# Kernel optimization log

Hardware: AMD Instinct MI355X
Metric: run time of the kernel (lower is better)

Reference implementation:

```python
import jax, jax.numpy as jnp
import numpy as np

H, W = 480, 640
NUM_CLASSES = 3
SKIP = 5            # skip_pixels: stride between voting pixels
GRID = 8            # stride of Hough accumulator bins
LABEL_THRESHOLD = 5
INLIER_THRESHOLD = 0.5
VOTING_THRESHOLD = 0.3


def setup_inputs():
    key = jax.random.key(0)
    k1, k2, k3, k4 = jax.random.split(key, 4)
    bottom_label = jax.random.randint(k1, (1, H, W), 0, NUM_CLASSES).astype(jnp.int32)
    bottom_vertex = jax.random.normal(k2, (1, NUM_CLASSES * 3, H, W), jnp.float32)
    bottom_meta_data = jax.random.normal(k3, (1, 10), jnp.float32)
    extents = jax.random.normal(k4, (NUM_CLASSES, 3), jnp.float32)
    return {"bottom_label": bottom_label, "bottom_vertex": bottom_vertex,
            "bottom_meta_data": bottom_meta_data, "extents": extents}


def _hough_voting(bottom_label, bottom_vertex, bottom_meta_data, extents):
    label = bottom_label[0]                                   # [H,W] int
    vert = bottom_vertex[0].reshape(NUM_CLASSES, 3, H, W)     # per-class (ux,uy,dist)

    # voter pixels on a SKIP-strided grid
    vy, vx = jnp.meshgrid(jnp.arange(0, H, SKIP), jnp.arange(0, W, SKIP), indexing="ij")
    vy = vy.reshape(-1)
    vx = vx.reshape(-1)                                       # [V]
    vl = label[vy, vx]                                        # voter class labels [V]
    d = vert[vl, :, vy, vx]                                   # [V,3] gather own-class prediction
    ux, uy, dist = d[:, 0], d[:, 1], d[:, 2]

    # Hough bin centers on a GRID-strided grid
    by, bx = jnp.meshgrid(jnp.arange(GRID // 2, H, GRID), jnp.arange(GRID // 2, W, GRID), indexing="ij")
    by = by.reshape(-1).astype(jnp.float32)
    bx = bx.reshape(-1).astype(jnp.float32)                   # [B]

    # per (voter, bin) agreement between predicted direction and vector to bin
    ddx = bx[None, :] - vx[:, None].astype(jnp.float32)       # [V,B]
    ddy = by[None, :] - vy[:, None].astype(jnp.float32)
    inv_n = jax.lax.rsqrt(ddx * ddx + ddy * ddy + 1e-6)
    cos = (ddx * ux[:, None] + ddy * uy[:, None]) * inv_n     # [V,B]
    w = jnp.where((cos > INLIER_THRESHOLD) & (vl[:, None] > 0), 1.0, 0.0)

    # scatter votes into per-class Hough space (class 0 = background, masked above)
    hough = jax.ops.segment_sum(w, vl, num_segments=NUM_CLASSES)                 # [C,B]
    dsum = jax.ops.segment_sum(w * dist[:, None], vl, num_segments=NUM_CLASSES)  # [C,B]
    counts = jax.ops.segment_sum(jnp.ones_like(vl, jnp.float32), vl, num_segments=NUM_CLASSES)

    # peak detection per class
    peak = jnp.argmax(hough, axis=1)                          # [C]
    votes = jnp.take_along_axis(hough, peak[:, None], axis=1)[:, 0]
    depth = jnp.take_along_axis(dsum, peak[:, None], axis=1)[:, 0] / jnp.maximum(votes, 1.0)
    cx = bx[peak]
    cy = by[peak]
    score = votes / jnp.maximum(counts, 1.0)
    valid = (counts > LABEL_THRESHOLD) & (score > VOTING_THRESHOLD)

    # project object extents through camera intrinsics at estimated depth -> box size
    fx = bottom_meta_data[0, 0]
    fy = bottom_meta_data[0, 4]
    diag = jnp.sqrt(jnp.sum(extents * extents, axis=1))       # [C]
    safe_z = jnp.maximum(jnp.abs(depth), 1e-3)
    bw = jnp.abs(diag * fx) / safe_z
    bh = jnp.abs(diag * fy) / safe_z

    cls = jnp.arange(NUM_CLASSES, dtype=jnp.float32)
    rois = jnp.stack([cls, cx - bw / 2, cy - bh / 2, cx + bw / 2, cy + bh / 2,
                      score * valid.astype(jnp.float32)], axis=1)  # [C,6]
    return rois, hough


def reference(bottom_label, bottom_vertex, bottom_meta_data, extents):
    return _hough_voting(bottom_label, bottom_vertex, bottom_meta_data, extents)
```

## Files before the change

kernel.cpp:

```cpp
#include <hip/hip_runtime.h>

#define HH 480
#define WW 640
#define NC 3
#define NVX 128
#define NVY 96
#define NV (NVX * NVY)
#define NBX 80
#define NBY 60
#define NB (NBX * NBY)
#define NPB 96
#define BKT 128
#define XBLK 10

__global__ void precompute_pts(const int* __restrict__ label,
                               const float* __restrict__ vert,
                               float4* __restrict__ ptsA,
                               float4* __restrict__ ptsB,
                               int* __restrict__ cnt,
                               float* __restrict__ blockCounts,
                               float* __restrict__ hough,
                               float* __restrict__ dsum) {
    __shared__ int swtot[2], sn2[2];
    const int tid = threadIdx.x;
    const int i = blockIdx.x * BKT + tid;
    const int iy = i >> 7;
    const int ix = i & (NVX - 1);
    const int pix = (5 * iy) * WW + 5 * ix;
    const int vl = label[pix];
    const float* base = vert + (size_t)(vl * 3) * HH * WW + pix;
    const float ux = base[0];
    const float uy = base[(size_t)HH * WW];
    const float dist = base[(size_t)2 * HH * WW];

    const bool pos = (vl > 0);
    const int lane = tid & 63, w = tid >> 6;
    unsigned long long mp = __ballot(pos);
    unsigned long long m2 = __ballot(vl == 2);
    int rank = __popcll(mp & ((1ull << lane) - 1ull));
    if (lane == 0) { swtot[w] = __popcll(mp); sn2[w] = __popcll(m2); }
    __syncthreads();
    if (pos) {
        int p = blockIdx.x * BKT + (w ? swtot[0] : 0) + rank;
        ptsA[p] = make_float4((float)(5 * ix), (float)(5 * iy), ux, uy);
        ptsB[p] = make_float4((vl == 1) ? dist : 0.0f,
                              (vl == 2) ? dist : 0.0f,
                              (vl == 1) ? 1.0f : 0.0f,
                              (vl == 2) ? 1.0f : 0.0f);
    }
    if (tid == 0) {
        int tot = swtot[0] + swtot[1];
        int n2 = sn2[0] + sn2[1];
        cnt[blockIdx.x] = tot;
        blockCounts[blockIdx.x * NC + 0] = (float)(BKT - tot);
        blockCounts[blockIdx.x * NC + 1] = (float)(tot - n2);
        blockCounts[blockIdx.x * NC + 2] = (float)n2;
    }
    for (int k = i; k < NC * NB; k += NV) hough[k] = 0.0f;
    if (i < 2 * NB) dsum[i] = 0.0f;
}

__global__ void vote(const float4* __restrict__ ptsA,
                     const float4* __restrict__ ptsB,
                     const int* __restrict__ cnt,
                     float* __restrict__ hough,
                     float* __restrict__ dsum) {
    __shared__ float4 shA[BKT];
    __shared__ float4 shB[BKT];
    const int tid = threadIdx.x;
    const int p0 = blockIdx.y * BKT;
    if (tid < BKT) shA[tid] = ptsA[p0 + tid];
    else           shB[tid - BKT] = ptsB[p0 + tid - BKT];
    const int n = cnt[blockIdx.y];

    const int b0 = 2 * (blockIdx.x * 256 + tid);
    const float bx0 = (float)(4 + 8 * (b0 % NBX));
    const float bx1 = bx0 + 8.0f;
    const float byf = (float)(4 + 8 * (b0 / NBX));
    float h10 = 0.f, h20 = 0.f, d10 = 0.f, d20 = 0.f;
    float h11 = 0.f, h21 = 0.f, d11 = 0.f, d21 = 0.f;
    float flagacc = -1.0f;
    __syncthreads();

    for (int j = 0; j < n; ++j) {
        float4 a = shA[j];
        float4 q = shB[j];
        float ddy = byf - a.y;
        float dyt = __builtin_fmaf(ddy, ddy, 1e-6f);
        float dyu = ddy * a.w;

        float ddx0 = bx0 - a.x;
        float nx0  = __builtin_fmaf(ddx0, ddx0, dyt);
        float dot0 = __builtin_fmaf(ddx0, a.z, dyu);
        float s0   = __builtin_fmaf(dot0, dot0, -0.25f * nx0);
        float g0   = fminf(dot0, s0);
        float f0   = fminf(dot0, __builtin_fmaf(nx0, 1e-6f, -fabsf(s0)));

        float ddx1 = bx1 - a.x;
        float nx1  = __builtin_fmaf(ddx1, ddx1, dyt);
        float dot1 = __builtin_fmaf(ddx1, a.z, dyu);
        float s1   = __builtin_fmaf(dot1, dot1, -0.25f * nx1);
        float g1   = fminf(dot1, s1);
        float f1   = fminf(dot1, __builtin_fmaf(nx1, 1e-6f, -fabsf(s1)));

        flagacc = fmaxf(flagacc, fmaxf(f0, f1));
        float m0 = (g0 > 0.0f) ? 1.0f : 0.0f;
        float m1 = (g1 > 0.0f) ? 1.0f : 0.0f;
        d10 = __builtin_fmaf(m0, q.x, d10);
        d20 = __builtin_fmaf(m0, q.y, d20);
        h10 = __builtin_fmaf(m0, q.z, h10);
        h20 = __builtin_fmaf(m0, q.w, h20);
        d11 = __builtin_fmaf(m1, q.x, d11);
        d21 = __builtin_fmaf(m1, q.y, d21);
        h11 = __builtin_fmaf(m1, q.z, h11);
        h21 = __builtin_fmaf(m1, q.w, h21);
    }

    if (b0 >= NB) flagacc = -1.0f;
    if (flagacc > 0.0f) {
        for (int j = 0; j < n; ++j) {
            float4 a = shA[j];
            float4 q = shB[j];
            float ddy = byf - a.y;
            float dyt = __builtin_fmaf(ddy, ddy, 1e-6f);
            float dyu = ddy * a.w;
#pragma unroll
            for (int k = 0; k < 2; ++k) {
                float bx = k ? bx1 : bx0;
                float ddx = bx - a.x;
                float nx  = __builtin_fmaf(ddx, ddx, dyt);
                float dot = __builtin_fmaf(ddx, a.z, dyu);
                float s   = __builtin_fmaf(dot, dot, -0.25f * nx);
                float mf  = (fminf(dot, s) > 0.0f) ? 1.0f : 0.0f;
                float nxe  = __fadd_rn(__fadd_rn(__fmul_rn(ddx, ddx),
                                                 __fmul_rn(ddy, ddy)), 1e-6f);
                float inve = __fdiv_rn(1.0f, __fsqrt_rn(nxe));
                float dote = __fadd_rn(__fmul_rn(ddx, a.z), __fmul_rn(ddy, a.w));
                float me   = (__fmul_rn(dote, inve) > 0.5f) ? 1.0f : 0.0f;
                float dm   = me - mf;
                if (k == 0) {
                    d10 = __builtin_fmaf(dm, q.x, d10);
                    d20 = __builtin_fmaf(dm, q.y, d20);
                    h10 = __builtin_fmaf(dm, q.z, h10);
                    h20 = __builtin_fmaf(dm, q.w, h20);
                } else {
                    d11 = __builtin_fmaf(dm, q.x, d11);
                    d21 = __builtin_fmaf(dm, q.y, d21);
                    h11 = __builtin_fmaf(dm, q.z, h11);
                    h21 = __builtin_fmaf(dm, q.w, h21);
                }
            }
        }
    }

    if (b0 < NB) {
        atomicAdd(&hough[NB + b0], h10);
        atomicAdd(&hough[2 * NB + b0], h20);
        atomicAdd(&dsum[b0], d10);
        atomicAdd(&dsum[NB + b0], d20);
        atomicAdd(&hough[NB + b0 + 1], h11);
        atomicAdd(&hough[2 * NB + b0 + 1], h21);
        atomicAdd(&dsum[b0 + 1], d11);
        atomicAdd(&dsum[NB + b0 + 1], d21);
    }
}

__global__ void finalize(const float* __restrict__ hough,
                         const float* __restrict__ dsum,
                         const float* __restrict__ blockCounts,
                         const float* __restrict__ meta,
                         const float* __restrict__ extents,
                         float* __restrict__ rois) {
    __shared__ unsigned long long skey[256];
    __shared__ float scnt[256];
    const int tid = threadIdx.x;
    const int c = blockIdx.x;

    float cntv = 0.0f;
    for (int i = tid; i < NPB; i += 256) cntv += blockCounts[i * NC + c];
    scnt[tid] = cntv;

    unsigned long long best = 0ull;
    for (int i = tid; i < NB; i += 256) {
        float v = hough[c * NB + i];
        unsigned long long key =
            ((unsigned long long)__float_as_uint(v) << 32) |
            (unsigned long long)(unsigned)(NB - 1 - i);
        if (key > best) best = key;
    }
    skey[tid] = best;
    __syncthreads();
    for (int s = 128; s > 0; s >>= 1) {
        if (tid < s) {
            if (skey[tid + s] > skey[tid]) skey[tid] = skey[tid + s];
            scnt[tid] += scnt[tid + s];
        }
        __syncthreads();
    }
    if (tid == 0) {
        float votes = __uint_as_float((unsigned)(skey[0] >> 32));
        int peak = NB - 1 - (int)(skey[0] & 0xffffffffull);
        float ds = (c == 0) ? 0.0f : dsum[(c - 1) * NB + peak];
        float depth = __fdiv_rn(ds, fmaxf(votes, 1.0f));
        float cx = (float)(4 + 8 * (peak % NBX));
        float cy = (float)(4 + 8 * (peak / NBX));
        float cntf = scnt[0];
        float score = __fdiv_rn(votes, fmaxf(cntf, 1.0f));
        int valid = (cntf > 5.0f) && (score > 0.3f);
        float fx = meta[0], fy = meta[4];
        float e0 = extents[c * 3 + 0];
        float e1 = extents[c * 3 + 1];
        float e2 = extents[c * 3 + 2];
        float diag = __fsqrt_rn(__fadd_rn(
            __fadd_rn(__fmul_rn(e0, e0), __fmul_rn(e1, e1)), __fmul_rn(e2, e2)));
        float sz = fmaxf(fabsf(depth), 0.001f);
        float bw = __fdiv_rn(fabsf(__fmul_rn(diag, fx)), sz);
        float bh = __fdiv_rn(fabsf(__fmul_rn(diag, fy)), sz);
        rois[c * 6 + 0] = (float)c;
        rois[c * 6 + 1] = cx - bw * 0.5f;
        rois[c * 6 + 2] = cy - bh * 0.5f;
        rois[c * 6 + 3] = cx + bw * 0.5f;
        rois[c * 6 + 4] = cy + bh * 0.5f;
        rois[c * 6 + 5] = valid ? score : 0.0f;
    }
}

extern "C" void kernel_launch(void* const* d_in, const int* in_sizes, int n_in,
                              void* d_out, int out_size, void* d_ws, size_t ws_size,
                              hipStream_t stream) {
    const int* label = (const int*)d_in[0];
    const float* vert = (const float*)d_in[1];
    const float* meta = (const float*)d_in[2];
    const float* extents = (const float*)d_in[3];
    float* out = (float*)d_out;

    char* ws = (char*)d_ws;
    float4* ptsA = (float4*)ws;
    float4* ptsB = (float4*)(ws + (size_t)NV * 16);
    float* dsum = (float*)(ws + (size_t)2 * NV * 16);
    float* blockCounts = (float*)(ws + (size_t)2 * NV * 16 + 2 * NB * 4);
    int* cnt = (int*)(ws + (size_t)2 * NV * 16 + 2 * NB * 4 + NPB * NC * 4);

    float* hough = out + NC * 6;

    precompute_pts<<<NPB, BKT, 0, stream>>>(label, vert, ptsA, ptsB,
                                            cnt, blockCounts, hough, dsum);
    vote<<<dim3(XBLK, NPB), 256, 0, stream>>>(ptsA, ptsB, cnt, hough, dsum);
    finalize<<<NC, 256, 0, stream>>>(hough, dsum, blockCounts, meta, extents, out);
}
```

Before: 113.0 us.

## Use 2x2 bin tiles per thread and replace atomics with partial-sum reduction

Each vote thread now handles a 2x2 block of Hough bins instead of a 1x2 pair, so the per-voter dy terms are reused across rows and only 5 x-blocks are launched. Global float atomics are replaced by per-voter-block partial planes written with float2 stores, and a new reduce kernel sums them. The zeroing of the hough and dsum buffers moves out of precompute into the reduce step. The cost is an extra kernel launch and roughly 7 MB of partial-buffer traffic, plus fewer threads in the vote kernel.

```diff
diff --git a/kernel.cpp b/kernel.cpp
--- a/kernel.cpp
+++ b/kernel.cpp
@@ -11,16 +11,15 @@
 #define NB (NBX * NBY)
 #define NPB 96
 #define BKT 128
-#define XBLK 10
+#define NLANE 1200
+#define XBLK 5
 
 __global__ void precompute_pts(const int* __restrict__ label,
                                const float* __restrict__ vert,
                                float4* __restrict__ ptsA,
                                float4* __restrict__ ptsB,
                                int* __restrict__ cnt,
-                               float* __restrict__ blockCounts,
-                               float* __restrict__ hough,
-                               float* __restrict__ dsum) {
+                               float* __restrict__ blockCounts) {
     __shared__ int swtot[2], sn2[2];
     const int tid = threadIdx.x;
     const int i = blockIdx.x * BKT + tid;
@@ -56,15 +55,12 @@
         blockCounts[blockIdx.x * NC + 1] = (float)(tot - n2);
         blockCounts[blockIdx.x * NC + 2] = (float)n2;
     }
-    for (int k = i; k < NC * NB; k += NV) hough[k] = 0.0f;
-    if (i < 2 * NB) dsum[i] = 0.0f;
 }
 
 __global__ void vote(const float4* __restrict__ ptsA,
                      const float4* __restrict__ ptsB,
                      const int* __restrict__ cnt,
-                     float* __restrict__ hough,
-                     float* __restrict__ dsum) {
+                     float* __restrict__ partial) {
     __shared__ float4 shA[BKT];
     __shared__ float4 shB[BKT];
     const int tid = threadIdx.x;
@@ -73,96 +69,115 @@
     else           shB[tid - BKT] = ptsB[p0 + tid - BKT];
     const int n = cnt[blockIdx.y];
 
-    const int b0 = 2 * (blockIdx.x * 256 + tid);
-    const float bx0 = (float)(4 + 8 * (b0 % NBX));
-    const float bx1 = bx0 + 8.0f;
-    const float byf = (float)(4 + 8 * (b0 / NBX));
-    float h10 = 0.f, h20 = 0.f, d10 = 0.f, d20 = 0.f;
-    float h11 = 0.f, h21 = 0.f, d11 = 0.f, d21 = 0.f;
+    const int gi = blockIdx.x * 256 + tid;
+    const int xp = gi % 40;
+    const int yp = gi / 40;
+    const float bx0 = (float)(4 + 16 * xp), bx1 = bx0 + 8.0f;
+    const float by0 = (float)(4 + 16 * yp), by1 = by0 + 8.0f;
+
+    float hh1[4] = {0.f, 0.f, 0.f, 0.f};
+    float hh2[4] = {0.f, 0.f, 0.f, 0.f};
+    float dd1[4] = {0.f, 0.f, 0.f, 0.f};
+    float dd2[4] = {0.f, 0.f, 0.f, 0.f};
     float flagacc = -1.0f;
     __syncthreads();
 
+#pragma unroll 2
     for (int j = 0; j < n; ++j) {
         float4 a = shA[j];
         float4 q = shB[j];
-        float ddy = byf - a.y;
-        float dyt = __builtin_fmaf(ddy, ddy, 1e-6f);
-        float dyu = ddy * a.w;
-
-        float ddx0 = bx0 - a.x;
-        float nx0  = __builtin_fmaf(ddx0, ddx0, dyt);
-        float dot0 = __builtin_fmaf(ddx0, a.z, dyu);
-        float s0   = __builtin_fmaf(dot0, dot0, -0.25f * nx0);
-        float g0   = fminf(dot0, s0);
-        float f0   = fminf(dot0, __builtin_fmaf(nx0, 1e-6f, -fabsf(s0)));
-
-        float ddx1 = bx1 - a.x;
-        float nx1  = __builtin_fmaf(ddx1, ddx1, dyt);
-        float dot1 = __builtin_fmaf(ddx1, a.z, dyu);
-        float s1   = __builtin_fmaf(dot1, dot1, -0.25f * nx1);
-        float g1   = fminf(dot1, s1);
-        float f1   = fminf(dot1, __builtin_fmaf(nx1, 1e-6f, -fabsf(s1)));
-
-        flagacc = fmaxf(flagacc, fmaxf(f0, f1));
-        float m0 = (g0 > 0.0f) ? 1.0f : 0.0f;
-        float m1 = (g1 > 0.0f) ? 1.0f : 0.0f;
-        d10 = __builtin_fmaf(m0, q.x, d10);
-        d20 = __builtin_fmaf(m0, q.y, d20);
-        h10 = __builtin_fmaf(m0, q.z, h10);
-        h20 = __builtin_fmaf(m0, q.w, h20);
-        d11 = __builtin_fmaf(m1, q.x, d11);
-        d21 = __builtin_fmaf(m1, q.y, d21);
-        h11 = __builtin_fmaf(m1, q.z, h11);
-        h21 = __builtin_fmaf(m1, q.w, h21);
-    }
-
-    if (b0 >= NB) flagacc = -1.0f;
+        float ddx[2] = {__fsub_rn(bx0, a.x), __fsub_rn(bx1, a.x)};
+        float ddy[2] = {__fsub_rn(by0, a.y), __fsub_rn(by1, a.y)};
+        float dxu[2], dyt[2], dyu[2];
+#pragma unroll
+        for (int c = 0; c < 2; ++c) dxu[c] = __fmul_rn(ddx[c], a.z);
+#pragma unroll
+        for (int r = 0; r < 2; ++r) {
+            dyt[r] = __builtin_fmaf(ddy[r], ddy[r], 1e-6f);
+            dyu[r] = __fmul_rn(ddy[r], a.w);
+        }
+#pragma unroll
+        for (int bb = 0; bb < 4; ++bb) {
+            const int r = bb >> 1, c = bb & 1;
+            float nx = __builtin_fmaf(ddx[c], ddx[c], dyt[r]);
+            float dt = __fadd_rn(dxu[c], dyu[r]);
+            float s  = __builtin_fmaf(dt, dt, __fmul_rn(-0.25f, nx));
+            float g  = fminf(dt, s);
+            float f  = fminf(dt, __builtin_fmaf(nx, 4e-6f, -fabsf(s)));
+            flagacc  = fmaxf(flagacc, f);
+            float m  = (g > 0.0f) ? 1.0f : 0.0f;
+            hh1[bb] = __builtin_fmaf(m, q.z, hh1[bb]);
+            hh2[bb] = __builtin_fmaf(m, q.w, hh2[bb]);
+            dd1[bb] = __builtin_fmaf(m, q.x, dd1[bb]);
+            dd2[bb] = __builtin_fmaf(m, q.y, dd2[bb]);
+        }
+    }
+
+    if (gi >= NLANE) flagacc = -1.0f;
     if (flagacc > 0.0f) {
         for (int j = 0; j < n; ++j) {
             float4 a = shA[j];
             float4 q = shB[j];
-            float ddy = byf - a.y;
-            float dyt = __builtin_fmaf(ddy, ddy, 1e-6f);
-            float dyu = ddy * a.w;
-#pragma unroll
-            for (int k = 0; k < 2; ++k) {
-                float bx = k ? bx1 : bx0;
-                float ddx = bx - a.x;
-                float nx  = __builtin_fmaf(ddx, ddx, dyt);
-                float dot = __builtin_fmaf(ddx, a.z, dyu);
-                float s   = __builtin_fmaf(dot, dot, -0.25f * nx);
-                float mf  = (fminf(dot, s) > 0.0f) ? 1.0f : 0.0f;
-                float nxe  = __fadd_rn(__fadd_rn(__fmul_rn(ddx, ddx),
-                                                 __fmul_rn(ddy, ddy)), 1e-6f);
+            float ddx[2] = {__fsub_rn(bx0, a.x), __fsub_rn(bx1, a.x)};
+            float ddy[2] = {__fsub_rn(by0, a.y), __fsub_rn(by1, a.y)};
+            float dxu[2], dyt[2], dyu[2];
+#pragma unroll
+            for (int c = 0; c < 2; ++c) dxu[c] = __fmul_rn(ddx[c], a.z);
+#pragma unroll
+            for (int r = 0; r < 2; ++r) {
+                dyt[r] = __builtin_fmaf(ddy[r], ddy[r], 1e-6f);
+                dyu[r] = __fmul_rn(ddy[r], a.w);
+            }
+#pragma unroll
+            for (int bb = 0; bb < 4; ++bb) {
+                const int r = bb >> 1, c = bb & 1;
+                float nx = __builtin_fmaf(ddx[c], ddx[c], dyt[r]);
+                float dt = __fadd_rn(dxu[c], dyu[r]);
+                float s  = __builtin_fmaf(dt, dt, __fmul_rn(-0.25f, nx));
+                float mf = (fminf(dt, s) > 0.0f) ? 1.0f : 0.0f;
+                float nxe  = __fadd_rn(__fadd_rn(__fmul_rn(ddx[c], ddx[c]),
+                                                 __fmul_rn(ddy[r], ddy[r])), 1e-6f);
                 float inve = __fdiv_rn(1.0f, __fsqrt_rn(nxe));
-                float dote = __fadd_rn(__fmul_rn(ddx, a.z), __fmul_rn(ddy, a.w));
+                float dote = __fadd_rn(__fmul_rn(ddx[c], a.z),
+                                       __fmul_rn(ddy[r], a.w));
                 float me   = (__fmul_rn(dote, inve) > 0.5f) ? 1.0f : 0.0f;
                 float dm   = me - mf;
-                if (k == 0) {
-                    d10 = __builtin_fmaf(dm, q.x, d10);
-                    d20 = __builtin_fmaf(dm, q.y, d20);
-                    h10 = __builtin_fmaf(dm, q.z, h10);
-                    h20 = __builtin_fmaf(dm, q.w, h20);
-                } else {
-                    d11 = __builtin_fmaf(dm, q.x, d11);
-                    d21 = __builtin_fmaf(dm, q.y, d21);
-                    h11 = __builtin_fmaf(dm, q.z, h11);
-                    h21 = __builtin_fmaf(dm, q.w, h21);
-                }
+                hh1[bb] = __builtin_fmaf(dm, q.z, hh1[bb]);
+                hh2[bb] = __builtin_fmaf(dm, q.w, hh2[bb]);
+                dd1[bb] = __builtin_fmaf(dm, q.x, dd1[bb]);
+                dd2[bb] = __builtin_fmaf(dm, q.y, dd2[bb]);
             }
         }
     }
 
-    if (b0 < NB) {
-        atomicAdd(&hough[NB + b0], h10);
-        atomicAdd(&hough[2 * NB + b0], h20);
-        atomicAdd(&dsum[b0], d10);
-        atomicAdd(&dsum[NB + b0], d20);
-        atomicAdd(&hough[NB + b0 + 1], h11);
-        atomicAdd(&hough[2 * NB + b0 + 1], h21);
-        atomicAdd(&dsum[b0 + 1], d11);
-        atomicAdd(&dsum[NB + b0 + 1], d21);
-    }
+    if (gi < NLANE) {
+        const int r0 = 2 * yp, c0 = 2 * xp;
+        float* base = partial + (size_t)blockIdx.y * 4 * NB;
+        *(float2*)&base[0 * NB + r0 * NBX + c0]       = make_float2(hh1[0], hh1[1]);
+        *(float2*)&base[0 * NB + (r0 + 1) * NBX + c0] = make_float2(hh1[2], hh1[3]);
+        *(float2*)&base[1 * NB + r0 * NBX + c0]       = make_float2(hh2[0], hh2[1]);
+        *(float2*)&base[1 * NB + (r0 + 1) * NBX + c0] = make_float2(hh2[2], hh2[3]);
+        *(float2*)&base[2 * NB + r0 * NBX + c0]       = make_float2(dd1[0], dd1[1]);
+        *(float2*)&base[2 * NB + (r0 + 1) * NBX + c0] = make_float2(dd1[2], dd1[3]);
+        *(float2*)&base[3 * NB + r0 * NBX + c0]       = make_float2(dd2[0], dd2[1]);
+        *(float2*)&base[3 * NB + (r0 + 1) * NBX + c0] = make_float2(dd2[2], dd2[3]);
+    }
+}
+
+__global__ void reduce(const float* __restrict__ partial,
+                       float* __restrict__ hough,
+                       float* __restrict__ dsum) {
+    const int t = blockIdx.x * 256 + threadIdx.x;
+    const int plane = t / NB;
+    const int b = t % NB;
+    const float* p = partial + plane * NB + b;
+    float s = 0.0f;
+#pragma unroll 8
+    for (int y = 0; y < NPB; ++y) s += p[(size_t)y * 4 * NB];
+    if (plane == 0) { hough[b] = 0.0f; hough[NB + b] = s; }
+    else if (plane == 1) hough[2 * NB + b] = s;
+    else if (plane == 2) dsum[b] = s;
+    else                 dsum[NB + b] = s;
 }
 
 __global__ void finalize(const float* __restrict__ hough,
@@ -235,16 +250,19 @@
     float* out = (float*)d_out;
 
     char* ws = (char*)d_ws;
-    float4* ptsA = (float4*)ws;
-    float4* ptsB = (float4*)(ws + (size_t)NV * 16);
-    float* dsum = (float*)(ws + (size_t)2 * NV * 16);
-    float* blockCounts = (float*)(ws + (size_t)2 * NV * 16 + 2 * NB * 4);
-    int* cnt = (int*)(ws + (size_t)2 * NV * 16 + 2 * NB * 4 + NPB * NC * 4);
+    size_t off = 0;
+    float4* ptsA = (float4*)(ws + off); off += (size_t)NV * 16;
+    float4* ptsB = (float4*)(ws + off); off += (size_t)NV * 16;
+    float* partial = (float*)(ws + off); off += (size_t)NPB * 4 * NB * 4;
+    float* dsum = (float*)(ws + off); off += (size_t)2 * NB * 4;
+    float* blockCounts = (float*)(ws + off); off += (size_t)NPB * NC * 4;
+    int* cnt = (int*)(ws + off);
 
     float* hough = out + NC * 6;
 
     precompute_pts<<<NPB, BKT, 0, stream>>>(label, vert, ptsA, ptsB,
-                                            cnt, blockCounts, hough, dsum);
-    vote<<<dim3(XBLK, NPB), 256, 0, stream>>>(ptsA, ptsB, cnt, hough, dsum);
+                                            cnt, blockCounts);
+    vote<<<dim3(XBLK, NPB), 256, 0, stream>>>(ptsA, ptsB, cnt, partial);
+    reduce<<<(4 * NB) / 256, 256, 0, stream>>>(partial, hough, dsum);
     finalize<<<NC, 256, 0, stream>>>(hough, dsum, blockCounts, meta, extents, out);
 }
```

Result: slower. 156.2 us (+38.3%).
